# Kernel optimization log

Hardware: AMD Instinct MI355X
Metric: run time of the kernel (lower is better)

Reference implementation:

```python
import math
import jax, jax.numpy as jnp
import numpy as np

G, PQ, PV = 12, 4, 8

def setup_inputs() -> dict:
    key = jax.random.key(0)
    ks = jax.random.split(key, 14)
    N, L, Cn, Ce, Ch = 1, 512, 384, 128, 192
    Node = jax.random.normal(ks[0], (N, L, Cn), jnp.float32)
    Edge = jax.random.normal(ks[1], (N, L, L, Ce), jnp.float32)
    # proper rotation matrices via QR of random gaussians
    raw = jax.random.normal(ks[2], (N, L, 3, 3), jnp.float32)
    rots, _ = jnp.linalg.qr(raw)
    trans = jax.random.normal(ks[3], (N, L, 3), jnp.float32) * 10.0
    def lin(k, fan_in, fan_out):
        return jax.random.normal(k, (fan_in, fan_out), jnp.float32) / np.sqrt(fan_in)
    return {
        'Node': Node, 'Edge': Edge, 'rots': rots, 'trans': trans,
        'Wq': lin(ks[4], Cn, Ch), 'Wk': lin(ks[5], Cn, Ch), 'Wv': lin(ks[6], Cn, Ch),
        'Wqv': lin(ks[7], Cn, 3 * G * PQ), 'Wkv': lin(ks[8], Cn, 3 * G * PQ),
        'Wvv': lin(ks[9], Cn, 3 * G * PV), 'Wbias': lin(ks[10], Ce, G),
        'gamma': jnp.zeros((G,), jnp.float32),
        'Wout': lin(ks[11], Ce * G + Ch + G * PV * 4, Cn),
        'bout': jnp.zeros((Cn,), jnp.float32),
    }

def reference(Node, Edge, rots, trans, Wq, Wk, Wv, Wqv, Wkv, Wvv, Wbias, gamma, Wout, bout):
    N, L, Cn = Node.shape
    Ce = Edge.shape[-1]
    Ch = Wq.shape[1]
    ppg = Ch // G
    t = trans / 10.0  # Frame(T.rots, T.trans / 10.0)
    q = (Node @ Wq).reshape(N, L, G, ppg)
    k = (Node @ Wk).reshape(N, L, G, ppg)
    v = (Node @ Wv).reshape(N, L, G, ppg)
    qv = (Node @ Wqv).reshape(N, L, G, PQ, 3)
    kv = (Node @ Wkv).reshape(N, L, G, PQ, 3)
    vv = (Node @ Wvv).reshape(N, L, G, PV, 3)
    apply_frame = lambda p: jnp.einsum('nlij,nlgpj->nlgpi', rots, p) + t[:, :, None, None]
    qv = apply_frame(qv)
    kv = apply_frame(kv)
    vv = apply_frame(vv)
    # pairwise squared point distances, summed over xyz and query points -> [N,L,L,G]
    d = qv[:, :, None] - kv[:, None]
    sq = jnp.sum(d * d, axis=(-1, -2))
    bias = jnp.einsum('nijc,cg->nijg', Edge, Wbias)
    WC = math.sqrt(2.0 / 9.0 / PQ)
    WL = math.sqrt(1.0 / 3.0)
    attn = jnp.einsum('nlgc,nmgc->nlmg', q, k) / math.sqrt(ppg) + bias
    attn = attn - jax.nn.softplus(gamma) * (WC / 2.0) * sq
    attn = jax.nn.softmax(WL * attn, axis=2)  # softmax over key index m
    O_Edge = jnp.einsum('nijg,nijc->nigc', attn, Edge).reshape(N, L, G * Ce)
    O_Node = jnp.einsum('nijg,njgc->nigc', attn, v).reshape(N, L, Ch)
    O_vec = jnp.einsum('nijg,njgpc->nigpc', attn, vv)
    # invert_apply: R^T (x - t)
    O_vec = jnp.einsum('nlji,nlgpj->nlgpi', rots, O_vec - t[:, :, None, None])
    O_norm = jnp.sqrt(jnp.sum(O_vec * O_vec, axis=-1) + 1e-8).reshape(N, L, -1)
    O_vec = O_vec.reshape(N, L, -1)
    feat = jnp.concatenate([O_Edge, O_Node, O_vec, O_norm], axis=-1)
    return feat @ Wout + bout
```

## Files before the change

kernel.cpp:

```cpp
#include <hip/hip_runtime.h>
#include <math.h>

#define LQ 512
#define CN 384
#define CE 128
#define CH 192
#define NG 12
#define PPG 16
#define FEAT 2112
#define NPROJ 1152

#define WS_RAW  0u
#define WS_QVG  589824u
#define WS_KVT  663552u
#define WS_VVG  737280u
#define WS_QN   884736u
#define WS_KNT  890880u
#define WS_KT   897024u
#define WS_ATT  995328u
#define WS_FEAT 4141056u
#define WS_PART 5222400u
#define WS_PM   WS_PART
#define WS_PS   (WS_PART + 12288u)

__global__ __launch_bounds__(256) void k1a_gemm(
    const float* __restrict__ Node,
    const float* __restrict__ Wq, const float* __restrict__ Wk,
    const float* __restrict__ Wv, const float* __restrict__ Wqv,
    const float* __restrict__ Wkv, const float* __restrict__ Wvv,
    float* __restrict__ ws)
{
    __shared__ float As[64][68];
    __shared__ float Bs[64][48];
    const int tid = threadIdx.x;
    const int cb = blockIdx.x % 24;
    const int l0 = (blockIdx.x / 24) * 64;
    const int col0 = cb * 48;

    const float* W; int nc, lc0;
    if (col0 < 192)      { W = Wq;  nc = 192; lc0 = col0; }
    else if (col0 < 384) { W = Wk;  nc = 192; lc0 = col0 - 192; }
    else if (col0 < 576) { W = Wv;  nc = 192; lc0 = col0 - 384; }
    else if (col0 < 720) { W = Wqv; nc = 144; lc0 = col0 - 576; }
    else if (col0 < 864) { W = Wkv; nc = 144; lc0 = col0 - 720; }
    else                 { W = Wvv; nc = 288; lc0 = col0 - 864; }

    const int tx = tid & 15, ty = tid >> 4;
    float acc[4][3];
#pragma unroll
    for (int r = 0; r < 4; ++r)
#pragma unroll
        for (int c = 0; c < 3; ++c) acc[r][c] = 0.f;

    for (int kc = 0; kc < 6; ++kc) {
        __syncthreads();
#pragma unroll
        for (int pass = 0; pass < 4; ++pass) {
            int m = (tid >> 4) + pass * 16;
            int kk = (tid & 15) * 4;
            const float4 a = *(const float4*)(Node + (size_t)(l0 + m) * CN + kc * 64 + kk);
            As[kk + 0][m] = a.x; As[kk + 1][m] = a.y;
            As[kk + 2][m] = a.z; As[kk + 3][m] = a.w;
        }
#pragma unroll
        for (int p = 0; p < 12; ++p) {
            int idx = p * 256 + tid;
            int kk = idx / 48, c = idx - kk * 48;
            Bs[kk][c] = W[(size_t)(kc * 64 + kk) * nc + lc0 + c];
        }
        __syncthreads();
#pragma unroll 8
        for (int kk = 0; kk < 64; ++kk) {
            const float4 av = *(const float4*)&As[kk][tx * 4];
            const float b0 = Bs[kk][ty * 3 + 0];
            const float b1 = Bs[kk][ty * 3 + 1];
            const float b2 = Bs[kk][ty * 3 + 2];
            acc[0][0] = fmaf(av.x, b0, acc[0][0]); acc[0][1] = fmaf(av.x, b1, acc[0][1]); acc[0][2] = fmaf(av.x, b2, acc[0][2]);
            acc[1][0] = fmaf(av.y, b0, acc[1][0]); acc[1][1] = fmaf(av.y, b1, acc[1][1]); acc[1][2] = fmaf(av.y, b2, acc[1][2]);
            acc[2][0] = fmaf(av.z, b0, acc[2][0]); acc[2][1] = fmaf(av.z, b1, acc[2][1]); acc[2][2] = fmaf(av.z, b2, acc[2][2]);
            acc[3][0] = fmaf(av.w, b0, acc[3][0]); acc[3][1] = fmaf(av.w, b1, acc[3][1]); acc[3][2] = fmaf(av.w, b2, acc[3][2]);
        }
    }
    float* raw = ws + WS_RAW;
#pragma unroll
    for (int r = 0; r < 4; ++r)
#pragma unroll
        for (int c = 0; c < 3; ++c)
            raw[(size_t)(l0 + tx * 4 + r) * NPROJ + col0 + ty * 3 + c] = acc[r][c];
    if (col0 >= 192 && col0 < 384) {
#pragma unroll
        for (int r = 0; r < 4; ++r)
#pragma unroll
            for (int c = 0; c < 3; ++c)
                ws[WS_KT + (size_t)(col0 - 192 + ty * 3 + c) * LQ + l0 + tx * 4 + r] = acc[r][c];
    }
}

__global__ __launch_bounds__(256) void k1b_vec(
    const float* __restrict__ rots, const float* __restrict__ trans,
    float* __restrict__ ws)
{
    __shared__ float sqbuf[96];
    const int tid = threadIdx.x;
    const int l = blockIdx.x;
    const float* raw = ws + WS_RAW + (size_t)l * NPROJ;

    if (tid < 192) {
        int src, pt, typ;
        if (tid < 48)      { typ = 0; pt = tid;      src = 576 + pt * 3; }
        else if (tid < 96) { typ = 1; pt = tid - 48; src = 720 + pt * 3; }
        else               { typ = 2; pt = tid - 96; src = 864 + pt * 3; }
        float v0 = raw[src], v1 = raw[src + 1], v2 = raw[src + 2];
        const float* R = rots + l * 9;
        float o0 = R[0] * v0 + R[1] * v1 + R[2] * v2 + trans[l * 3 + 0] * 0.1f;
        float o1 = R[3] * v0 + R[4] * v1 + R[5] * v2 + trans[l * 3 + 1] * 0.1f;
        float o2 = R[6] * v0 + R[7] * v1 + R[8] * v2 + trans[l * 3 + 2] * 0.1f;
        if (typ == 0) {
            float* dst = ws + WS_QVG + (size_t)l * 144 + pt * 3;
            dst[0] = o0; dst[1] = o1; dst[2] = o2;
        } else if (typ == 1) {
            ws[WS_KVT + (size_t)(pt * 3 + 0) * LQ + l] = o0;
            ws[WS_KVT + (size_t)(pt * 3 + 1) * LQ + l] = o1;
            ws[WS_KVT + (size_t)(pt * 3 + 2) * LQ + l] = o2;
        } else {
            float* dst = ws + WS_VVG + (size_t)l * 288 + pt * 3;
            dst[0] = o0; dst[1] = o1; dst[2] = o2;
        }
        if (tid < 96) sqbuf[tid] = o0 * o0 + o1 * o1 + o2 * o2;
    }
    __syncthreads();
    if (tid < 24) {
        int typ = tid / 12, g = tid % 12;
        int b = typ * 48 + g * 4;
        float s = sqbuf[b] + sqbuf[b + 1] + sqbuf[b + 2] + sqbuf[b + 3];
        if (typ == 0) ws[WS_QN + (size_t)l * 12 + g] = s;
        else          ws[WS_KNT + (size_t)g * LQ + l] = s;
    }
}

__global__ __launch_bounds__(256, 4) void k2_attn(
    const float* __restrict__ Edge, const float* __restrict__ Wbias,
    const float* __restrict__ gamma, float* __restrict__ ws)
{
    __shared__ float et[256 * 33];
    __shared__ float cgls[NG];
    __shared__ float red[4][NG];
    const int tid = threadIdx.x;
    const int i = blockIdx.x >> 1;
    const int h = blockIdx.x & 1;
    const int j = h * 256 + tid;

    if (tid < NG)
        cgls[tid] = log1pf(__expf(gamma[tid])) * 0.11785113019775793f;
    __syncthreads();

    float lgs[NG];
    {
        const float* qrow  = ws + WS_RAW + (size_t)i * NPROJ;
        const float* qvrow = ws + WS_QVG + (size_t)i * 144;
        const float* qnrow = ws + WS_QN  + (size_t)i * NG;
        const float* KT  = ws + WS_KT;
        const float* KVT = ws + WS_KVT;
        const float* KNT = ws + WS_KNT;
#pragma unroll
        for (int g = 0; g < NG; ++g) {
            float qk = 0.f;
#pragma unroll
            for (int u = 0; u < PPG; ++u)
                qk = fmaf(qrow[g * PPG + u], KT[(size_t)(g * PPG + u) * LQ + j], qk);
            float dt = 0.f;
#pragma unroll
            for (int u = 0; u < 12; ++u)
                dt = fmaf(qvrow[g * 12 + u], KVT[(size_t)(g * 12 + u) * LQ + j], dt);
            float sq = qnrow[g] + KNT[(size_t)g * LQ + j] - 2.f * dt;
            lgs[g] = qk * 0.25f - cgls[g] * sq;
        }
    }

    const float4* e4 = (const float4*)Edge + ((size_t)i * LQ + h * 256) * 32;
    for (int ch = 0; ch < 4; ++ch) {
        __syncthreads();
#pragma unroll
        for (int kk = 0; kk < 8; ++kk) {
            int idx = kk * 256 + tid;
            int jr = idx >> 3, c4 = idx & 7;
            float4 v = e4[(size_t)jr * 32 + ch * 8 + c4];
            float* d = et + jr * 33 + c4 * 4;
            d[0] = v.x; d[1] = v.y; d[2] = v.z; d[3] = v.w;
        }
        __syncthreads();
        const float* wbch = Wbias + ch * 32 * NG;
        const float* r0 = et + tid * 33;
#pragma unroll 4
        for (int c = 0; c < 32; ++c) {
            float e0 = r0[c];
            const float* wb = wbch + c * NG;
#pragma unroll
            for (int g = 0; g < NG; ++g) lgs[g] = fmaf(e0, wb[g], lgs[g]);
        }
    }

    const float WL = 0.5773502691896258f;
    const int wid = tid >> 6, lane = tid & 63;
    float pm[NG];
#pragma unroll
    for (int g = 0; g < NG; ++g) pm[g] = lgs[g];
#pragma unroll
    for (int g = 0; g < NG; ++g)
        for (int off = 1; off < 64; off <<= 1)
            pm[g] = fmaxf(pm[g], __shfl_xor(pm[g], off));
    if (lane == 0) {
#pragma unroll
        for (int g = 0; g < NG; ++g) red[wid][g] = pm[g];
    }
    __syncthreads();
    float gm[NG];
#pragma unroll
    for (int g = 0; g < NG; ++g)
        gm[g] = fmaxf(fmaxf(red[0][g], red[1][g]), fmaxf(red[2][g], red[3][g]));
    if (tid < NG)
        ws[WS_PM + ((size_t)i * 2 + h) * NG + tid] =
            fmaxf(fmaxf(red[0][tid], red[1][tid]), fmaxf(red[2][tid], red[3][tid]));
    __syncthreads();

    float ps[NG];
#pragma unroll
    for (int g = 0; g < NG; ++g) {
        float e = __expf(WL * (lgs[g] - gm[g]));
        lgs[g] = e;
        ps[g] = e;
    }
#pragma unroll
    for (int g = 0; g < NG; ++g)
        for (int off = 1; off < 64; off <<= 1)
            ps[g] += __shfl_xor(ps[g], off);
    if (lane == 0) {
#pragma unroll
        for (int g = 0; g < NG; ++g) red[wid][g] = ps[g];
    }
    __syncthreads();
    if (tid < NG)
        ws[WS_PS + ((size_t)i * 2 + h) * NG + tid] =
            red[0][tid] + red[1][tid] + red[2][tid] + red[3][tid];

    float4* dst = (float4*)(ws + WS_ATT + ((size_t)i * LQ + j) * NG);
    float4 s0, s1, s2;
    s0.x = lgs[0]; s0.y = lgs[1]; s0.z = lgs[2];  s0.w = lgs[3];
    s1.x = lgs[4]; s1.y = lgs[5]; s1.z = lgs[6];  s1.w = lgs[7];
    s2.x = lgs[8]; s2.y = lgs[9]; s2.z = lgs[10]; s2.w = lgs[11];
    dst[0] = s0; dst[1] = s1; dst[2] = s2;
}

__global__ __launch_bounds__(256) void k3_out(
    const float* __restrict__ Edge, const float* __restrict__ rots,
    const float* __restrict__ trans, float* __restrict__ ws)
{
    __shared__ float at[LQ][13];
    __shared__ float bufA[4][32][NG][4];
    __shared__ float ovec[288];
    __shared__ float sc[2][NG];
    const int tid = threadIdx.x;
    const int qi = blockIdx.x;
    const float* att = ws + WS_ATT + (size_t)qi * LQ * NG;

    if (tid < 24) {
        const float WL = 0.5773502691896258f;
        int hh = tid / NG, g = tid % NG;
        float m0 = ws[WS_PM + ((size_t)qi * 2 + 0) * NG + g];
        float m1 = ws[WS_PM + ((size_t)qi * 2 + 1) * NG + g];
        float ss0 = ws[WS_PS + ((size_t)qi * 2 + 0) * NG + g];
        float ss1 = ws[WS_PS + ((size_t)qi * 2 + 1) * NG + g];
        float m = fmaxf(m0, m1);
        float e0 = __expf(WL * (m0 - m));
        float e1 = __expf(WL * (m1 - m));
        float denom = ss0 * e0 + ss1 * e1;
        sc[hh][g] = (hh ? e1 : e0) / denom;
    }
    __syncthreads();

    for (int m = 0; m < 2; ++m) {
        int j = tid + m * 256;
        int hh = j >> 8;
        const float4* src = (const float4*)(att + (size_t)j * NG);
        float4 a = src[0], b = src[1], c = src[2];
        at[j][0] = a.x * sc[hh][0]; at[j][1] = a.y * sc[hh][1];
        at[j][2] = a.z * sc[hh][2]; at[j][3] = a.w * sc[hh][3];
        at[j][4] = b.x * sc[hh][4]; at[j][5] = b.y * sc[hh][5];
        at[j][6] = b.z * sc[hh][6]; at[j][7] = b.w * sc[hh][7];
        at[j][8] = c.x * sc[hh][8]; at[j][9] = c.y * sc[hh][9];
        at[j][10] = c.z * sc[hh][10]; at[j][11] = c.w * sc[hh][11];
    }
    __syncthreads();

    const int w = tid >> 6, lane = tid & 63, jh = lane >> 5, c4 = lane & 31;
    float acc[NG][4];
#pragma unroll
    for (int g = 0; g < NG; ++g)
#pragma unroll
        for (int r = 0; r < 4; ++r) acc[g][r] = 0.f;
    const float4* e4 = (const float4*)(Edge + (size_t)qi * LQ * CE);
    for (int jj = 0; jj < 64; ++jj) {
        int j = w * 128 + jh * 64 + jj;
        float4 e = e4[(size_t)j * 32 + c4];
#pragma unroll
        for (int g = 0; g < NG; ++g) {
            float a = at[j][g];
            acc[g][0] = fmaf(a, e.x, acc[g][0]);
            acc[g][1] = fmaf(a, e.y, acc[g][1]);
            acc[g][2] = fmaf(a, e.z, acc[g][2]);
            acc[g][3] = fmaf(a, e.w, acc[g][3]);
        }
    }
#pragma unroll
    for (int g = 0; g < NG; ++g)
#pragma unroll
        for (int r = 0; r < 4; ++r) acc[g][r] += __shfl_xor(acc[g][r], 32);
    if (jh == 0) {
#pragma unroll
        for (int g = 0; g < NG; ++g)
#pragma unroll
            for (int r = 0; r < 4; ++r) bufA[w][c4][g][r] = acc[g][r];
    }
    __syncthreads();
    float* feat = ws + WS_FEAT + (size_t)qi * FEAT;
    for (int m = 0; m < 6; ++m) {
        int o = tid + m * 256;
        int g = o >> 7, c = o & 127;
        int cc4 = c >> 2, r = c & 3;
        feat[o] = bufA[0][cc4][g][r] + bufA[1][cc4][g][r] +
                  bufA[2][cc4][g][r] + bufA[3][cc4][g][r];
    }

    const float* raw = ws + WS_RAW;
    const float* vvg = ws + WS_VVG;
    for (int ph = 0; ph < 2; ++ph) {
        int task = tid + ph * 256;
        if (task < 192) {
            int g = task >> 4;
            float s = 0.f;
            for (int j = 0; j < LQ; ++j) s = fmaf(at[j][g], raw[(size_t)j * NPROJ + 384 + task], s);
            feat[1536 + task] = s;
        } else if (task < 480) {
            int u = task - 192;
            int g = u / 24;
            float s = 0.f;
            for (int j = 0; j < LQ; ++j) s = fmaf(at[j][g], vvg[(size_t)j * 288 + u], s);
            ovec[u] = s;
        }
    }
    __syncthreads();

    if (tid < 96) {
        int g = tid >> 3, p = tid & 7;
        const float* R = rots + qi * 9;
        float t0 = trans[qi * 3 + 0] * 0.1f;
        float t1 = trans[qi * 3 + 1] * 0.1f;
        float t2 = trans[qi * 3 + 2] * 0.1f;
        float d0 = ovec[g * 24 + p * 3 + 0] - t0;
        float d1 = ovec[g * 24 + p * 3 + 1] - t1;
        float d2 = ovec[g * 24 + p * 3 + 2] - t2;
        float o0 = R[0] * d0 + R[3] * d1 + R[6] * d2;
        float o1 = R[1] * d0 + R[4] * d1 + R[7] * d2;
        float o2 = R[2] * d0 + R[5] * d1 + R[8] * d2;
        feat[1728 + g * 24 + p * 3 + 0] = o0;
        feat[1728 + g * 24 + p * 3 + 1] = o1;
        feat[1728 + g * 24 + p * 3 + 2] = o2;
        feat[2016 + g * 8 + p] = sqrtf(o0 * o0 + o1 * o1 + o2 * o2 + 1e-8f);
    }
}

__global__ __launch_bounds__(256) void k4_gemm(const float* __restrict__ Wout,
                                               float* __restrict__ ws)
{
    __shared__ float As[64][68];
    __shared__ float Bs[64][48];
    const int tid = threadIdx.x;
    const int cc = blockIdx.x >> 6;
    const int t  = blockIdx.x & 63;
    const int l0 = (t >> 3) * 64;
    const int col0 = (t & 7) * 48;
    const float* feat = ws + WS_FEAT;

    const int tx = tid & 15, ty = tid >> 4;
    float acc[4][3];
#pragma unroll
    for (int r = 0; r < 4; ++r)
#pragma unroll
        for (int c = 0; c < 3; ++c) acc[r][c] = 0.f;

    for (int kc = cc * 11; kc < cc * 11 + 11; ++kc) {
        __syncthreads();
#pragma unroll
        for (int pass = 0; pass < 4; ++pass) {
            int m = (tid >> 4) + pass * 16;
            int kk = (tid & 15) * 4;
            const float4 a = *(const float4*)(feat + (size_t)(l0 + m) * FEAT + kc * 64 + kk);
            As[kk + 0][m] = a.x; As[kk + 1][m] = a.y;
            As[kk + 2][m] = a.z; As[kk + 3][m] = a.w;
        }
#pragma unroll
        for (int p = 0; p < 12; ++p) {
            int idx = p * 256 + tid;
            int kk = idx / 48, c = idx - kk * 48;
            Bs[kk][c] = Wout[(size_t)(kc * 64 + kk) * CN + col0 + c];
        }
        __syncthreads();
#pragma unroll 8
        for (int kk = 0; kk < 64; ++kk) {
            const float4 av = *(const float4*)&As[kk][tx * 4];
            const float b0 = Bs[kk][ty * 3 + 0];
            const float b1 = Bs[kk][ty * 3 + 1];
            const float b2 = Bs[kk][ty * 3 + 2];
            acc[0][0] = fmaf(av.x, b0, acc[0][0]); acc[0][1] = fmaf(av.x, b1, acc[0][1]); acc[0][2] = fmaf(av.x, b2, acc[0][2]);
            acc[1][0] = fmaf(av.y, b0, acc[1][0]); acc[1][1] = fmaf(av.y, b1, acc[1][1]); acc[1][2] = fmaf(av.y, b2, acc[1][2]);
            acc[2][0] = fmaf(av.z, b0, acc[2][0]); acc[2][1] = fmaf(av.z, b1, acc[2][1]); acc[2][2] = fmaf(av.z, b2, acc[2][2]);
            acc[3][0] = fmaf(av.w, b0, acc[3][0]); acc[3][1] = fmaf(av.w, b1, acc[3][1]); acc[3][2] = fmaf(av.w, b2, acc[3][2]);
        }
    }
    float* part = ws + WS_PART + (size_t)cc * LQ * CN;
#pragma unroll
    for (int r = 0; r < 4; ++r)
#pragma unroll
        for (int c = 0; c < 3; ++c)
            part[(size_t)(l0 + tx * 4 + r) * CN + col0 + ty * 3 + c] = acc[r][c];
}

__global__ __launch_bounds__(384) void k5_red(const float* __restrict__ bout,
                                              const float* __restrict__ wsc,
                                              float* __restrict__ out)
{
    const int i = blockIdx.x, n = threadIdx.x;
    const float* part = wsc + WS_PART;
    size_t idx = (size_t)i * CN + n;
    size_t st = (size_t)LQ * CN;
    out[idx] = part[idx] + part[st + idx] + part[2 * st + idx] + bout[n];
}

extern "C" void kernel_launch(void* const* d_in, const int* in_sizes, int n_in,
                              void* d_out, int out_size, void* d_ws, size_t ws_size,
                              hipStream_t stream) {
    const float* Node  = (const float*)d_in[0];
    const float* Edge  = (const float*)d_in[1];
    const float* rots  = (const float*)d_in[2];
    const float* trans = (const float*)d_in[3];
    const float* Wq    = (const float*)d_in[4];
    const float* Wk    = (const float*)d_in[5];
    const float* Wv    = (const float*)d_in[6];
    const float* Wqv   = (const float*)d_in[7];
    const float* Wkv   = (const float*)d_in[8];
    const float* Wvv   = (const float*)d_in[9];
    const float* Wbias = (const float*)d_in[10];
    const float* gamma = (const float*)d_in[11];
    const float* Wout  = (const float*)d_in[12];
    const float* bout  = (const float*)d_in[13];
    float* ws = (float*)d_ws;

    k1a_gemm<<<192, 256, 0, stream>>>(Node, Wq, Wk, Wv, Wqv, Wkv, Wvv, ws);
    k1b_vec<<<512, 256, 0, stream>>>(rots, trans, ws);
    k2_attn<<<1024, 256, 0, stream>>>(Edge, Wbias, gamma, ws);
    k3_out<<<512, 256, 0, stream>>>(Edge, rots, trans, ws);
    k4_gemm<<<192, 256, 0, stream>>>(Wout, ws);
    k5_red<<<512, 384, 0, stream>>>(bout, ws, (float*)d_out);
}
```

Before: 202.0 us.

## Split attention and output kernels, double-buffer Edge tiles, transpose attention layout

```diff
diff --git a/kernel.cpp b/kernel.cpp
--- a/kernel.cpp
+++ b/kernel.cpp
@@ -9,6 +9,7 @@
 #define PPG 16
 #define FEAT 2112
 #define NPROJ 1152
+#define WLs 0.5773502691896258f
 
 #define WS_RAW  0u
 #define WS_QVG  589824u
@@ -20,8 +21,9 @@
 #define WS_ATT  995328u
 #define WS_FEAT 4141056u
 #define WS_PART 5222400u
-#define WS_PM   WS_PART
-#define WS_PS   (WS_PART + 12288u)
+#define WS_PM   5812224u
+#define WS_PS   5824512u
+#define WS_LGS  5861376u
 
 __global__ __launch_bounds__(256) void k1a_gemm(
     const float* __restrict__ Node,
@@ -138,13 +140,10 @@
     }
 }
 
-__global__ __launch_bounds__(256, 4) void k2_attn(
-    const float* __restrict__ Edge, const float* __restrict__ Wbias,
+__global__ __launch_bounds__(256) void k2a_logits(
     const float* __restrict__ gamma, float* __restrict__ ws)
 {
-    __shared__ float et[256 * 33];
     __shared__ float cgls[NG];
-    __shared__ float red[4][NG];
     const int tid = threadIdx.x;
     const int i = blockIdx.x >> 1;
     const int h = blockIdx.x & 1;
@@ -154,43 +153,81 @@
         cgls[tid] = log1pf(__expf(gamma[tid])) * 0.11785113019775793f;
     __syncthreads();
 
+    const float* qrow  = ws + WS_RAW + (size_t)i * NPROJ;
+    const float* qvrow = ws + WS_QVG + (size_t)i * 144;
+    const float* qnrow = ws + WS_QN  + (size_t)i * NG;
+    const float* KT  = ws + WS_KT;
+    const float* KVT = ws + WS_KVT;
+    const float* KNT = ws + WS_KNT;
+    float lgs[NG];
+#pragma unroll
+    for (int g = 0; g < NG; ++g) {
+        float qk = 0.f;
+#pragma unroll
+        for (int u = 0; u < PPG; ++u)
+            qk = fmaf(qrow[g * PPG + u], KT[(size_t)(g * PPG + u) * LQ + j], qk);
+        float dt = 0.f;
+#pragma unroll
+        for (int u = 0; u < 12; ++u)
+            dt = fmaf(qvrow[g * 12 + u], KVT[(size_t)(g * 12 + u) * LQ + j], dt);
+        float sq = qnrow[g] + KNT[(size_t)g * LQ + j] - 2.f * dt;
+        lgs[g] = qk * 0.25f - cgls[g] * sq;
+    }
+    float4* dst = (float4*)(ws + WS_LGS + ((size_t)i * LQ + j) * NG);
+    float4 s0, s1, s2;
+    s0.x = lgs[0]; s0.y = lgs[1]; s0.z = lgs[2];  s0.w = lgs[3];
+    s1.x = lgs[4]; s1.y = lgs[5]; s1.z = lgs[6];  s1.w = lgs[7];
+    s2.x = lgs[8]; s2.y = lgs[9]; s2.z = lgs[10]; s2.w = lgs[11];
+    dst[0] = s0; dst[1] = s1; dst[2] = s2;
+}
+
+__global__ __launch_bounds__(256, 2) void k2b_bias(
+    const float* __restrict__ Edge, const float* __restrict__ Wbias,
+    float* __restrict__ ws)
+{
+    __shared__ float et[2][256 * 33];
+    __shared__ float red[4][NG];
+    const int tid = threadIdx.x;
+    const int i = blockIdx.x >> 1;
+    const int h = blockIdx.x & 1;
+    const int j = h * 256 + tid;
+    const int jr = tid >> 3, c4s = tid & 7;
+
     float lgs[NG];
     {
-        const float* qrow  = ws + WS_RAW + (size_t)i * NPROJ;
-        const float* qvrow = ws + WS_QVG + (size_t)i * 144;
-        const float* qnrow = ws + WS_QN  + (size_t)i * NG;
-        const float* KT  = ws + WS_KT;
-        const float* KVT = ws + WS_KVT;
-        const float* KNT = ws + WS_KNT;
-#pragma unroll
-        for (int g = 0; g < NG; ++g) {
-            float qk = 0.f;
-#pragma unroll
-            for (int u = 0; u < PPG; ++u)
-                qk = fmaf(qrow[g * PPG + u], KT[(size_t)(g * PPG + u) * LQ + j], qk);
-            float dt = 0.f;
-#pragma unroll
-            for (int u = 0; u < 12; ++u)
-                dt = fmaf(qvrow[g * 12 + u], KVT[(size_t)(g * 12 + u) * LQ + j], dt);
-            float sq = qnrow[g] + KNT[(size_t)g * LQ + j] - 2.f * dt;
-            lgs[g] = qk * 0.25f - cgls[g] * sq;
-        }
+        const float4* lg4 = (const float4*)(ws + WS_LGS + ((size_t)i * LQ + j) * NG);
+        float4 L0 = lg4[0], L1 = lg4[1], L2 = lg4[2];
+        lgs[0] = L0.x; lgs[1] = L0.y; lgs[2] = L0.z;  lgs[3] = L0.w;
+        lgs[4] = L1.x; lgs[5] = L1.y; lgs[6] = L1.z;  lgs[7] = L1.w;
+        lgs[8] = L2.x; lgs[9] = L2.y; lgs[10] = L2.z; lgs[11] = L2.w;
     }
 
     const float4* e4 = (const float4*)Edge + ((size_t)i * LQ + h * 256) * 32;
+    float4 buf[8];
+
+#pragma unroll
+    for (int kk = 0; kk < 8; ++kk) {
+        int idx = kk * 256 + tid;
+        buf[kk] = e4[(size_t)(idx >> 3) * 32 + (idx & 7)];
+    }
+#pragma unroll
+    for (int kk = 0; kk < 8; ++kk) {
+        int idx = kk * 256 + tid;
+        float* d = et[0] + (idx >> 3) * 33 + (idx & 7) * 4;
+        d[0] = buf[kk].x; d[1] = buf[kk].y; d[2] = buf[kk].z; d[3] = buf[kk].w;
+    }
+    __syncthreads();
+
     for (int ch = 0; ch < 4; ++ch) {
-        __syncthreads();
-#pragma unroll
-        for (int kk = 0; kk < 8; ++kk) {
-            int idx = kk * 256 + tid;
-            int jr = idx >> 3, c4 = idx & 7;
-            float4 v = e4[(size_t)jr * 32 + ch * 8 + c4];
-            float* d = et + jr * 33 + c4 * 4;
-            d[0] = v.x; d[1] = v.y; d[2] = v.z; d[3] = v.w;
-        }
-        __syncthreads();
+        if (ch < 3) {
+#pragma unroll
+            for (int kk = 0; kk < 8; ++kk) {
+                int idx = kk * 256 + tid;
+                buf[kk] = e4[(size_t)(idx >> 3) * 32 + (ch + 1) * 8 + (idx & 7)];
+            }
+        }
         const float* wbch = Wbias + ch * 32 * NG;
-        const float* r0 = et + tid * 33;
+        const float* r0 = et[ch & 1] + tid * 33;
 #pragma unroll 4
         for (int c = 0; c < 32; ++c) {
             float e0 = r0[c];
@@ -198,9 +235,17 @@
 #pragma unroll
             for (int g = 0; g < NG; ++g) lgs[g] = fmaf(e0, wb[g], lgs[g]);
         }
-    }
-
-    const float WL = 0.5773502691896258f;
+        if (ch < 3) {
+#pragma unroll
+            for (int kk = 0; kk < 8; ++kk) {
+                int idx = kk * 256 + tid;
+                float* d = et[(ch + 1) & 1] + (idx >> 3) * 33 + (idx & 7) * 4;
+                d[0] = buf[kk].x; d[1] = buf[kk].y; d[2] = buf[kk].z; d[3] = buf[kk].w;
+            }
+        }
+        __syncthreads();
+    }
+
     const int wid = tid >> 6, lane = tid & 63;
     float pm[NG];
 #pragma unroll
@@ -226,7 +271,7 @@
     float ps[NG];
 #pragma unroll
     for (int g = 0; g < NG; ++g) {
-        float e = __expf(WL * (lgs[g] - gm[g]));
+        float e = __expf(WLs * (lgs[g] - gm[g]));
         lgs[g] = e;
         ps[g] = e;
     }
@@ -243,52 +288,43 @@
         ws[WS_PS + ((size_t)i * 2 + h) * NG + tid] =
             red[0][tid] + red[1][tid] + red[2][tid] + red[3][tid];
 
-    float4* dst = (float4*)(ws + WS_ATT + ((size_t)i * LQ + j) * NG);
-    float4 s0, s1, s2;
-    s0.x = lgs[0]; s0.y = lgs[1]; s0.z = lgs[2];  s0.w = lgs[3];
-    s1.x = lgs[4]; s1.y = lgs[5]; s1.z = lgs[6];  s1.w = lgs[7];
-    s2.x = lgs[8]; s2.y = lgs[9]; s2.z = lgs[10]; s2.w = lgs[11];
-    dst[0] = s0; dst[1] = s1; dst[2] = s2;
-}
-
-__global__ __launch_bounds__(256) void k3_out(
-    const float* __restrict__ Edge, const float* __restrict__ rots,
-    const float* __restrict__ trans, float* __restrict__ ws)
-{
-    __shared__ float at[LQ][13];
+    float* attT = ws + WS_ATT + (size_t)i * (NG * LQ);
+#pragma unroll
+    for (int g = 0; g < NG; ++g) attT[g * LQ + j] = lgs[g];
+}
+
+__global__ __launch_bounds__(256) void k3a_oedge(
+    const float* __restrict__ Edge, float* __restrict__ ws)
+{
+    __shared__ float atls[NG * 516];
     __shared__ float bufA[4][32][NG][4];
-    __shared__ float ovec[288];
     __shared__ float sc[2][NG];
     const int tid = threadIdx.x;
     const int qi = blockIdx.x;
-    const float* att = ws + WS_ATT + (size_t)qi * LQ * NG;
 
     if (tid < 24) {
-        const float WL = 0.5773502691896258f;
         int hh = tid / NG, g = tid % NG;
         float m0 = ws[WS_PM + ((size_t)qi * 2 + 0) * NG + g];
         float m1 = ws[WS_PM + ((size_t)qi * 2 + 1) * NG + g];
         float ss0 = ws[WS_PS + ((size_t)qi * 2 + 0) * NG + g];
         float ss1 = ws[WS_PS + ((size_t)qi * 2 + 1) * NG + g];
         float m = fmaxf(m0, m1);
-        float e0 = __expf(WL * (m0 - m));
-        float e1 = __expf(WL * (m1 - m));
+        float e0 = __expf(WLs * (m0 - m));
+        float e1 = __expf(WLs * (m1 - m));
         float denom = ss0 * e0 + ss1 * e1;
         sc[hh][g] = (hh ? e1 : e0) / denom;
     }
     __syncthreads();
 
-    for (int m = 0; m < 2; ++m) {
-        int j = tid + m * 256;
-        int hh = j >> 8;
-        const float4* src = (const float4*)(att + (size_t)j * NG);
-        float4 a = src[0], b = src[1], c = src[2];
-        at[j][0] = a.x * sc[hh][0]; at[j][1] = a.y * sc[hh][1];
-        at[j][2] = a.z * sc[hh][2]; at[j][3] = a.w * sc[hh][3];
-        at[j][4] = b.x * sc[hh][4]; at[j][5] = b.y * sc[hh][5];
-        at[j][6] = b.z * sc[hh][6]; at[j][7] = b.w * sc[hh][7];
-        at[j][8] = c.x * sc[hh][8]; at[j][9] = c.y * sc[hh][9];
-        at[j][10] = c.z * sc[hh][10]; at[j][11] = c.w * sc[hh][11];
+    const float4* attT4 = (const float4*)(ws + WS_ATT + (size_t)qi * (NG * LQ));
+#pragma unroll
+    for (int m = 0; m < 6; ++m) {
+        int idx = m * 256 + tid;
+        int g = idx >> 7, j4 = idx & 127;
+        float s = sc[j4 >> 6][g];
+        float4 v = attT4[g * 128 + j4];
+        v.x *= s; v.y *= s; v.z *= s; v.w *= s;
+        *(float4*)&atls[g * 516 + j4 * 4] = v;
     }
     __syncthreads();
 
@@ -299,16 +335,19 @@
 #pragma unroll
         for (int r = 0; r < 4; ++r) acc[g][r] = 0.f;
     const float4* e4 = (const float4*)(Edge + (size_t)qi * LQ * CE);
-    for (int jj = 0; jj < 64; ++jj) {
-        int j = w * 128 + jh * 64 + jj;
-        float4 e = e4[(size_t)j * 32 + c4];
+    for (int s = 0; s < 16; ++s) {
+        int j0 = w * 128 + jh * 64 + s * 4;
+        float4 e0 = e4[(size_t)(j0 + 0) * 32 + c4];
+        float4 e1 = e4[(size_t)(j0 + 1) * 32 + c4];
+        float4 e2 = e4[(size_t)(j0 + 2) * 32 + c4];
+        float4 e3 = e4[(size_t)(j0 + 3) * 32 + c4];
 #pragma unroll
         for (int g = 0; g < NG; ++g) {
-            float a = at[j][g];
-            acc[g][0] = fmaf(a, e.x, acc[g][0]);
-            acc[g][1] = fmaf(a, e.y, acc[g][1]);
-            acc[g][2] = fmaf(a, e.z, acc[g][2]);
-            acc[g][3] = fmaf(a, e.w, acc[g][3]);
+            float4 a = *(const float4*)&atls[g * 516 + j0];
+            acc[g][0] = fmaf(a.x, e0.x, fmaf(a.y, e1.x, fmaf(a.z, e2.x, fmaf(a.w, e3.x, acc[g][0]))));
+            acc[g][1] = fmaf(a.x, e0.y, fmaf(a.y, e1.y, fmaf(a.z, e2.y, fmaf(a.w, e3.y, acc[g][1]))));
+            acc[g][2] = fmaf(a.x, e0.z, fmaf(a.y, e1.z, fmaf(a.z, e2.z, fmaf(a.w, e3.z, acc[g][2]))));
+            acc[g][3] = fmaf(a.x, e0.w, fmaf(a.y, e1.w, fmaf(a.z, e2.w, fmaf(a.w, e3.w, acc[g][3]))));
         }
     }
 #pragma unroll
@@ -330,42 +369,99 @@
         feat[o] = bufA[0][cc4][g][r] + bufA[1][cc4][g][r] +
                   bufA[2][cc4][g][r] + bufA[3][cc4][g][r];
     }
-
+}
+
+__global__ __launch_bounds__(256) void k3b_rest(
+    const float* __restrict__ rots, const float* __restrict__ trans,
+    float* __restrict__ ws)
+{
+    __shared__ float atls[NG * 516];
+    __shared__ float sc[2][NG];
+    __shared__ float ovecl[240];
+    const int tid = threadIdx.x;
+    const int qi = blockIdx.x >> 1;
+    const int s  = blockIdx.x & 1;
+
+    if (tid < 24) {
+        int hh = tid / NG, g = tid % NG;
+        float m0 = ws[WS_PM + ((size_t)qi * 2 + 0) * NG + g];
+        float m1 = ws[WS_PM + ((size_t)qi * 2 + 1) * NG + g];
+        float ss0 = ws[WS_PS + ((size_t)qi * 2 + 0) * NG + g];
+        float ss1 = ws[WS_PS + ((size_t)qi * 2 + 1) * NG + g];
+        float m = fmaxf(m0, m1);
+        float e0 = __expf(WLs * (m0 - m));
+        float e1 = __expf(WLs * (m1 - m));
+        float denom = ss0 * e0 + ss1 * e1;
+        sc[hh][g] = (hh ? e1 : e0) / denom;
+    }
+    __syncthreads();
+
+    const float4* attT4 = (const float4*)(ws + WS_ATT + (size_t)qi * (NG * LQ));
+#pragma unroll
+    for (int m = 0; m < 6; ++m) {
+        int idx = m * 256 + tid;
+        int g = idx >> 7, j4 = idx & 127;
+        float f = sc[j4 >> 6][g];
+        float4 v = attT4[g * 128 + j4];
+        v.x *= f; v.y *= f; v.z *= f; v.w *= f;
+        *(float4*)&atls[g * 516 + j4 * 4] = v;
+    }
+    __syncthreads();
+
+    float* feat = ws + WS_FEAT + (size_t)qi * FEAT;
     const float* raw = ws + WS_RAW;
     const float* vvg = ws + WS_VVG;
-    for (int ph = 0; ph < 2; ++ph) {
-        int task = tid + ph * 256;
-        if (task < 192) {
-            int g = task >> 4;
-            float s = 0.f;
-            for (int j = 0; j < LQ; ++j) s = fmaf(at[j][g], raw[(size_t)j * NPROJ + 384 + task], s);
-            feat[1536 + task] = s;
-        } else if (task < 480) {
-            int u = task - 192;
+    if (tid < 240) {
+        if (s == 0 && tid < 192) {
+            int g = tid >> 4;
+            const float* arow = atls + g * 516;
+            float sum = 0.f;
+            for (int j4 = 0; j4 < 128; ++j4) {
+                float4 a = *(const float4*)&arow[j4 * 4];
+                int j = j4 * 4;
+                sum = fmaf(a.x, raw[(size_t)(j + 0) * NPROJ + 384 + tid], sum);
+                sum = fmaf(a.y, raw[(size_t)(j + 1) * NPROJ + 384 + tid], sum);
+                sum = fmaf(a.z, raw[(size_t)(j + 2) * NPROJ + 384 + tid], sum);
+                sum = fmaf(a.w, raw[(size_t)(j + 3) * NPROJ + 384 + tid], sum);
+            }
+            feat[1536 + tid] = sum;
+        } else {
+            int u = (s == 0) ? (tid - 192) : (48 + tid);
+            int lidx = (s == 0) ? (tid - 192) : tid;
             int g = u / 24;
-            float s = 0.f;
-            for (int j = 0; j < LQ; ++j) s = fmaf(at[j][g], vvg[(size_t)j * 288 + u], s);
-            ovec[u] = s;
-        }
-    }
-    __syncthreads();
-
-    if (tid < 96) {
-        int g = tid >> 3, p = tid & 7;
+            const float* arow = atls + g * 516;
+            float sum = 0.f;
+            for (int j4 = 0; j4 < 128; ++j4) {
+                float4 a = *(const float4*)&arow[j4 * 4];
+                int j = j4 * 4;
+                sum = fmaf(a.x, vvg[(size_t)(j + 0) * 288 + u], sum);
+                sum = fmaf(a.y, vvg[(size_t)(j + 1) * 288 + u], sum);
+                sum = fmaf(a.z, vvg[(size_t)(j + 2) * 288 + u], sum);
+                sum = fmaf(a.w, vvg[(size_t)(j + 3) * 288 + u], sum);
+            }
+            ovecl[lidx] = sum;
+        }
+    }
+    __syncthreads();
+
+    int npts = (s == 0) ? 16 : 80;
+    if (tid < npts) {
+        int P = (s == 0) ? tid : (16 + tid);
+        int u0l = (s == 0) ? (P * 3) : (P * 3 - 48);
         const float* R = rots + qi * 9;
         float t0 = trans[qi * 3 + 0] * 0.1f;
         float t1 = trans[qi * 3 + 1] * 0.1f;
         float t2 = trans[qi * 3 + 2] * 0.1f;
-        float d0 = ovec[g * 24 + p * 3 + 0] - t0;
-        float d1 = ovec[g * 24 + p * 3 + 1] - t1;
-        float d2 = ovec[g * 24 + p * 3 + 2] - t2;
+        float d0 = ovecl[u0l + 0] - t0;
+        float d1 = ovecl[u0l + 1] - t1;
+        float d2 = ovecl[u0l + 2] - t2;
         float o0 = R[0] * d0 + R[3] * d1 + R[6] * d2;
         float o1 = R[1] * d0 + R[4] * d1 + R[7] * d2;
         float o2 = R[2] * d0 + R[5] * d1 + R[8] * d2;
-        feat[1728 + g * 24 + p * 3 + 0] = o0;
-        feat[1728 + g * 24 + p * 3 + 1] = o1;
-        feat[1728 + g * 24 + p * 3 + 2] = o2;
-        feat[2016 + g * 8 + p] = sqrtf(o0 * o0 + o1 * o1 + o2 * o2 + 1e-8f);
+        feat[1728 + P * 3 + 0] = o0;
+        feat[1728 + P * 3 + 1] = o1;
+        feat[1728 + P * 3 + 2] = o2;
+        feat[2016 + P] = sqrtf(o0 * o0 + o1 * o1 + o2 * o2 + 1e-8f);
     }
 }
 
@@ -457,8 +553,10 @@
 
     k1a_gemm<<<192, 256, 0, stream>>>(Node, Wq, Wk, Wv, Wqv, Wkv, Wvv, ws);
     k1b_vec<<<512, 256, 0, stream>>>(rots, trans, ws);
-    k2_attn<<<1024, 256, 0, stream>>>(Edge, Wbias, gamma, ws);
-    k3_out<<<512, 256, 0, stream>>>(Edge, rots, trans, ws);
+    k2a_logits<<<1024, 256, 0, stream>>>(gamma, ws);
+    k2b_bias<<<1024, 256, 0, stream>>>(Edge, Wbias, ws);
+    k3a_oedge<<<512, 256, 0, stream>>>(Edge, ws);
+    k3b_rest<<<1024, 256, 0, stream>>>(rots, trans, ws);
     k4_gemm<<<192, 256, 0, stream>>>(Wout, ws);
     k5_red<<<512, 384, 0, stream>>>(bout, ws, (float*)d_out);
 }
```

New measurement: 208.0 us. 1.03x slower.
